# Kernel tuning notes

Hardware: AMD Instinct MI355X
Metric: run time of the kernel (lower is better)

The kernel has to match this reference:

```python
import jax, jax.numpy as jnp
import numpy as np

C = 256
HEADS = 8
HEAD_DIM = C // HEADS
GROUPS = 8
EPS = 1e-5


def setup_inputs() -> dict:
    key = jax.random.key(0)
    ks = jax.random.split(key, 11)
    B, S = 2, 16
    s = 0.02
    return {
        "x": jax.random.normal(ks[0], (B, C, S, S, S), dtype=jnp.float32),
        "gn_w": jnp.ones((C,), jnp.float32),
        "gn_b": jnp.zeros((C,), jnp.float32),
        "wq": jax.random.normal(ks[1], (C, C), jnp.float32) * s,
        "bq": jnp.zeros((C,), jnp.float32),
        "wk": jax.random.normal(ks[2], (C, C), jnp.float32) * s,
        "bk": jnp.zeros((C,), jnp.float32),
        "wv": jax.random.normal(ks[3], (C, C), jnp.float32) * s,
        "bv": jnp.zeros((C,), jnp.float32),
        "wo": jax.random.normal(ks[4], (C, C), jnp.float32) * s,
        "bo": jnp.zeros((C,), jnp.float32),
    }


def _group_norm(x, w, b):
    # x: [B, C, D, H, W]; GroupNorm(8, C) with affine params
    B, Cc, D, H, W = x.shape
    xg = x.reshape(B, GROUPS, Cc // GROUPS, D, H, W)
    mu = jnp.mean(xg, axis=(2, 3, 4, 5), keepdims=True)
    var = jnp.mean(jnp.square(xg - mu), axis=(2, 3, 4, 5), keepdims=True)
    xn = ((xg - mu) * jax.lax.rsqrt(var + EPS)).reshape(B, Cc, D, H, W)
    return xn * w[None, :, None, None, None] + b[None, :, None, None, None]


def reference(x, gn_w, gn_b, wq, bq, wk, bk, wv, bv, wo, bo):
    B, Cc, D, H, W = x.shape
    N = D * H * W
    xn = _group_norm(x, gn_w, gn_b).reshape(B, Cc, N)  # [B,C,N]
    # 1x1x1 Conv3d == per-voxel linear: weight [out,in]
    Q = jnp.einsum("oc,bcn->bon", wq, xn) + bq[None, :, None]
    K = jnp.einsum("oc,bcn->bon", wk, xn) + bk[None, :, None]
    V = jnp.einsum("oc,bcn->bon", wv, xn) + bv[None, :, None]
    Q = Q.reshape(B, HEADS, HEAD_DIM, N)
    K = K.reshape(B, HEADS, HEAD_DIM, N)
    V = V.reshape(B, HEADS, HEAD_DIM, N)
    scale = np.sqrt(HEAD_DIM).astype(np.float32)
    attn = jnp.einsum("bhdn,bhdm->bhnm", Q, K) / scale
    attn = jax.nn.softmax(attn, axis=-1)
    out = jnp.einsum("bhnm,bhdm->bhdn", attn, V)  # [B,h,hd,N]
    out = out.reshape(B, Cc, N)
    out = jnp.einsum("oc,bcn->bon", wo, out) + bo[None, :, None]
    return x + out.reshape(B, Cc, D, H, W)
```

## Files before the change

### kernel.cpp

```cpp
#include <hip/hip_runtime.h>

#define B_   2
#define C_   256
#define N_   4096
#define H_   8
#define HD_  32
#define G_   8
#define CPG_ 32

typedef short short8 __attribute__((ext_vector_type(8)));
typedef short short4v __attribute__((ext_vector_type(4)));
typedef unsigned uint4v __attribute__((ext_vector_type(4)));
typedef float f32x4  __attribute__((ext_vector_type(4)));
typedef float f4     __attribute__((ext_vector_type(4)));

__device__ __forceinline__ float b2f(short s) {
    return __uint_as_float(((unsigned)(unsigned short)s) << 16);
}
__device__ __forceinline__ short f2b(float f) {
    unsigned u = __float_as_uint(f);
    unsigned r = (u + 0x7FFF + ((u >> 16) & 1)) >> 16;
    return (short)r;
}

__global__ __launch_bounds__(256) void gn_part(const float* __restrict__ x,
                                               float* __restrict__ part) {
    int blk = blockIdx.x;
    const f4* p = (const f4*)x + (size_t)(blk >> 6) * (CPG_ * N_ / 4) + (size_t)(blk & 63) * 512;
    float s = 0.f, ss = 0.f;
#pragma unroll
    for (int i = 0; i < 2; i++) {
        f4 v = p[threadIdx.x + i * 256];
#pragma unroll
        for (int j = 0; j < 4; j++) { float f = v[j]; s += f; ss += f * f; }
    }
#pragma unroll
    for (int off = 32; off > 0; off >>= 1) {
        s  += __shfl_down(s, off);
        ss += __shfl_down(ss, off);
    }
    __shared__ float rs[4], rss[4];
    int w = threadIdx.x >> 6;
    if ((threadIdx.x & 63) == 0) { rs[w] = s; rss[w] = ss; }
    __syncthreads();
    if (threadIdx.x == 0) {
        part[blk * 2]     = rs[0] + rs[1] + rs[2] + rs[3];
        part[blk * 2 + 1] = rss[0] + rss[1] + rss[2] + rss[3];
    }
}

__global__ __launch_bounds__(256) void gemm_qkv(
    const float* __restrict__ x,
    const float* __restrict__ gw, const float* __restrict__ gb,
    const float* __restrict__ part,
    const float* __restrict__ wq, const float* __restrict__ bq,
    const float* __restrict__ wk, const float* __restrict__ bk,
    const float* __restrict__ wv, const float* __restrict__ bv,
    short* __restrict__ q, short* __restrict__ kt, short* __restrict__ v) {
    int z = blockIdx.z;
    int b = z / 3, which = z % 3;
    const float* W    = which == 0 ? wq : (which == 1 ? wk : wv);
    const float* bias = which == 0 ? bq : (which == 1 ? bk : bv);
    bool trans = (which != 2);
    float mul = (which == 0) ? (0.17677669529663687f * 1.4426950408889634f) : 1.0f;

    __shared__ short wl[64][40];
    __shared__ short xl[128][40];
    __shared__ float ga[256], gbb[256];
    __shared__ float mus[8], rstds[8];

    int o0 = blockIdx.y * 64, n0 = blockIdx.x * 128;
    int tid = threadIdx.x;
    int w = tid >> 6, lane = tid & 63, li = lane & 15, quad = lane >> 4;
    int wr = w & 1, wc = w >> 1;

#pragma unroll
    for (int gi = 0; gi < 2; gi++) {
        int g = w * 2 + gi;
        const float* pp = &part[(size_t)(b * 8 + g) * 128 + lane * 2];
        float s = pp[0], ss = pp[1];
#pragma unroll
        for (int off = 32; off > 0; off >>= 1) {
            s  += __shfl_down(s, off);
            ss += __shfl_down(ss, off);
        }
        if (lane == 0) {
            const float inv = 1.f / (float)(CPG_ * N_);
            float mu = s * inv;
            float var = ss * inv - mu * mu;
            mus[g] = mu;
            rstds[g] = rsqrtf(var + 1e-5f);
        }
    }
    __syncthreads();
    {
        int c = tid, g = c >> 5;
        float a = rstds[g] * gw[c];
        ga[c]  = a;
        gbb[c] = gb[c] - mus[g] * a;
    }

    f32x4 acc[8];
#pragma unroll
    for (int i = 0; i < 8; i++) acc[i] = (f32x4){0.f, 0.f, 0.f, 0.f};

    int cpair = tid >> 4, l16 = tid & 15;
    __syncthreads();

    for (int k0 = 0; k0 < 256; k0 += 32) {
        {
            int row = tid >> 2, co = (tid & 3) << 3;
            const float* wp = &W[(size_t)(o0 + row) * 256 + k0 + co];
            f4 wa = *(const f4*)wp;
            f4 wb = *(const f4*)(wp + 4);
            short8 w8;
#pragma unroll
            for (int j = 0; j < 4; j++) { w8[j] = f2b(wa[j]); w8[j + 4] = f2b(wb[j]); }
            *(short8*)&wl[row][co] = w8;
        }
        {
            int c0 = k0 + cpair * 2;
            float a0 = ga[c0],     b0c = gbb[c0];
            float a1 = ga[c0 + 1], b1c = gbb[c0 + 1];
            const float* xr0 = x + ((size_t)(b * 256 + c0)) * N_ + n0 + l16;
            const float* xr1 = xr0 + N_;
#pragma unroll
            for (int j = 0; j < 8; j++) {
                unsigned lo = (unsigned short)f2b(xr0[16 * j] * a0 + b0c);
                unsigned hi = (unsigned short)f2b(xr1[16 * j] * a1 + b1c);
                *(unsigned*)&xl[l16 + 16 * j][cpair * 2] = lo | (hi << 16);
            }
        }
        __syncthreads();
        short8 af[4], bfr[4];
        if (trans) {
#pragma unroll
            for (int i = 0; i < 4; i++) af[i]  = *(short8*)&xl[wr * 64 + i * 16 + li][quad * 8];
#pragma unroll
            for (int j = 0; j < 2; j++) bfr[j] = *(short8*)&wl[wc * 32 + j * 16 + li][quad * 8];
#pragma unroll
            for (int i = 0; i < 4; i++)
#pragma unroll
                for (int j = 0; j < 2; j++)
                    acc[i * 2 + j] = __builtin_amdgcn_mfma_f32_16x16x32_bf16(af[i], bfr[j], acc[i * 2 + j], 0, 0, 0);
        } else {
#pragma unroll
            for (int i = 0; i < 2; i++) af[i]  = *(short8*)&wl[wr * 32 + i * 16 + li][quad * 8];
#pragma unroll
            for (int j = 0; j < 4; j++) bfr[j] = *(short8*)&xl[wc * 64 + j * 16 + li][quad * 8];
#pragma unroll
            for (int i = 0; i < 2; i++)
#pragma unroll
                for (int j = 0; j < 4; j++)
                    acc[i * 4 + j] = __builtin_amdgcn_mfma_f32_16x16x32_bf16(af[i], bfr[j], acc[i * 4 + j], 0, 0, 0);
        }
        __syncthreads();
    }

    if (which == 2) {
        short* outp = v + (size_t)b * C_ * N_;
#pragma unroll
        for (int i = 0; i < 2; i++) {
            int ob = o0 + wr * 32 + i * 16 + quad * 4;
#pragma unroll
            for (int j = 0; j < 4; j++) {
                int n_ = n0 + wc * 64 + j * 16 + li;
#pragma unroll
                for (int r = 0; r < 4; r++) {
                    float val = acc[i * 4 + j][r] + bias[ob + r];
                    outp[(size_t)(ob + r) * N_ + n_] = f2b(val);
                }
            }
        }
    } else if (which == 0) {
        short* outp = q + (size_t)b * N_ * C_;
#pragma unroll
        for (int i = 0; i < 4; i++) {
            int nb_ = n0 + wr * 64 + i * 16 + quad * 4;
#pragma unroll
            for (int j = 0; j < 2; j++) {
                int o_ = o0 + wc * 32 + j * 16 + li;
                float bv_ = bias[o_];
#pragma unroll
                for (int r = 0; r < 4; r++)
                    outp[(size_t)(nb_ + r) * C_ + o_] = f2b((acc[i * 2 + j][r] + bv_) * mul);
            }
        }
    } else {
#pragma unroll
        for (int i = 0; i < 4; i++) {
            int nb_ = n0 + wr * 64 + i * 16 + quad * 4;
#pragma unroll
            for (int j = 0; j < 2; j++) {
                int o_ = o0 + wc * 32 + j * 16 + li;
                int hh = o_ >> 5, d = o_ & 31;
                float bv_ = bias[o_];
                short* kdst = kt + ((size_t)(b * 8 + hh) * N_) * HD_ + d;
#pragma unroll
                for (int r = 0; r < 4; r++)
                    kdst[(size_t)(nb_ + r) * HD_] = f2b(acc[i * 2 + j][r] + bv_);
            }
        }
    }
}

__global__ __launch_bounds__(512) void flash(const short* __restrict__ q,
                                             const short* __restrict__ ktp,
                                             const short* __restrict__ v,
                                             float* __restrict__ Opart,
                                             float* __restrict__ lrbuf) {
    int bid = blockIdx.x;
    int xcd = bid & 7;
    int rest = bid >> 3;
    int bh = xcd * 2 + (rest & 1);
    int r2 = rest >> 1;
    int nb = r2 & 15;
    int half = r2 >> 4;
    int b = bh >> 3, h = bh & 7;

    const short* QT = q   + (size_t)b * N_ * C_ + h * HD_;
    const short* KP = ktp + (size_t)bh * N_ * HD_ + (size_t)half * 2048 * HD_;
    const short* V  = v   + ((size_t)b * C_ + h * HD_) * N_ + half * 2048;
    float* Oh  = Opart + (size_t)half * B_ * N_ * C_ + (size_t)b * N_ * C_ + h * HD_;
    float* lrp = lrbuf + (size_t)half * 16 * N_ + (size_t)bh * N_;

    __shared__ short kl[2 * 2560];
    __shared__ short vl[2 * 2304];

    int tid = threadIdx.x, w = tid >> 6, lane = tid & 63, li = lane & 15, quad = lane >> 4;
    int n0w = nb * 256 + w * 32;

    short8 qf0 = *(const short8*)&QT[(size_t)(n0w + li) * 256 + quad * 8];
    short8 qf1 = *(const short8*)&QT[(size_t)(n0w + 16 + li) * 256 + quad * 8];

    f32x4 oa00 = (f32x4){0.f,0.f,0.f,0.f}, oa01 = oa00, oa10 = oa00, oa11 = oa00;
    float lr0 = 0.f, lr1 = 0.f;
    const f32x4 zero = (f32x4){0.f, 0.f, 0.f, 0.f};

    int krow = tid >> 3, kcol = (tid & 7) << 2;
    const short* kgp = KP + (size_t)krow * HD_ + kcol;
    int klo = krow * 40 + kcol;
    int vd = tid >> 4, g = tid & 15;
    int mbase = 32 * (g >> 3) + 16 * (g & 1) + 4 * ((g >> 1) & 3);
    const short* vgp = V + (size_t)vd * N_ + mbase;
    int vlo = vd * 72 + g * 4;

    short4v kst = *(const short4v*)kgp;
    short4v vst = *(const short4v*)vgp;

    f32x4 s0[4], s1[4];
    short8 vf[4];

    for (int t = 0; t < 32; ++t) {
        int buf = t & 1;
        *(short4v*)&kl[buf * 2560 + klo] = kst;
        *(short4v*)&vl[buf * 2304 + vlo] = vst;
        if (t < 31) {
            kst = *(const short4v*)(kgp + (size_t)(t + 1) * 64 * HD_);
            vst = *(const short4v*)(vgp + (t + 1) * 64);
        }
        __syncthreads();

        __builtin_amdgcn_s_setprio(1);
#pragma unroll
        for (int c = 0; c < 4; c++) {
            short8 kf = *(short8*)&kl[buf * 2560 + (c * 16 + li) * 40 + quad * 8];
            s0[c] = __builtin_amdgcn_mfma_f32_16x16x32_bf16(kf, qf0, zero, 0, 0, 0);
            s1[c] = __builtin_amdgcn_mfma_f32_16x16x32_bf16(kf, qf1, zero, 0, 0, 0);
        }
        __builtin_amdgcn_s_setprio(0);

        vf[0] = *(short8*)&vl[buf * 2304 + li * 72 + quad * 8];
        vf[1] = *(short8*)&vl[buf * 2304 + (16 + li) * 72 + quad * 8];
        vf[2] = *(short8*)&vl[buf * 2304 + li * 72 + 32 + quad * 8];
        vf[3] = *(short8*)&vl[buf * 2304 + (16 + li) * 72 + 32 + quad * 8];

        unsigned paw[8];
        float lp = 0.f;
#pragma unroll
        for (int c = 0; c < 4; c++) {
            float e0 = __builtin_amdgcn_exp2f(s0[c][0]);
            float e1 = __builtin_amdgcn_exp2f(s0[c][1]);
            float e2 = __builtin_amdgcn_exp2f(s0[c][2]);
            float e3 = __builtin_amdgcn_exp2f(s0[c][3]);
            lp += (e0 + e1) + (e2 + e3);
            paw[2 * c]     = __builtin_amdgcn_perm(__float_as_uint(e1), __float_as_uint(e0), 0x07060302);
            paw[2 * c + 1] = __builtin_amdgcn_perm(__float_as_uint(e3), __float_as_uint(e2), 0x07060302);
        }
        lr0 += lp;
        uint4v p0 = (uint4v){paw[0], paw[1], paw[2], paw[3]};
        uint4v p1 = (uint4v){paw[4], paw[5], paw[6], paw[7]};
        short8 a0 = __builtin_bit_cast(short8, p0);
        short8 a1 = __builtin_bit_cast(short8, p1);

        lp = 0.f;
#pragma unroll
        for (int c = 0; c < 4; c++) {
            float e0 = __builtin_amdgcn_exp2f(s1[c][0]);
            float e1 = __builtin_amdgcn_exp2f(s1[c][1]);
            float e2 = __builtin_amdgcn_exp2f(s1[c][2]);
            float e3 = __builtin_amdgcn_exp2f(s1[c][3]);
            lp += (e0 + e1) + (e2 + e3);
            paw[2 * c]     = __builtin_amdgcn_perm(__float_as_uint(e1), __float_as_uint(e0), 0x07060302);
            paw[2 * c + 1] = __builtin_amdgcn_perm(__float_as_uint(e3), __float_as_uint(e2), 0x07060302);
        }
        lr1 += lp;
        uint4v p2 = (uint4v){paw[0], paw[1], paw[2], paw[3]};
        uint4v p3 = (uint4v){paw[4], paw[5], paw[6], paw[7]};
        short8 a2 = __builtin_bit_cast(short8, p2);
        short8 a3 = __builtin_bit_cast(short8, p3);

        __builtin_amdgcn_s_setprio(1);
        oa00 = __builtin_amdgcn_mfma_f32_16x16x32_bf16(a0, vf[0], oa00, 0, 0, 0);
        oa01 = __builtin_amdgcn_mfma_f32_16x16x32_bf16(a0, vf[1], oa01, 0, 0, 0);
        oa00 = __builtin_amdgcn_mfma_f32_16x16x32_bf16(a1, vf[2], oa00, 0, 0, 0);
        oa01 = __builtin_amdgcn_mfma_f32_16x16x32_bf16(a1, vf[3], oa01, 0, 0, 0);
        oa10 = __builtin_amdgcn_mfma_f32_16x16x32_bf16(a2, vf[0], oa10, 0, 0, 0);
        oa11 = __builtin_amdgcn_mfma_f32_16x16x32_bf16(a2, vf[1], oa11, 0, 0, 0);
        oa10 = __builtin_amdgcn_mfma_f32_16x16x32_bf16(a3, vf[2], oa10, 0, 0, 0);
        oa11 = __builtin_amdgcn_mfma_f32_16x16x32_bf16(a3, vf[3], oa11, 0, 0, 0);
        __builtin_amdgcn_s_setprio(0);
    }

    lr0 += __shfl_xor(lr0, 16); lr0 += __shfl_xor(lr0, 32);
    lr1 += __shfl_xor(lr1, 16); lr1 += __shfl_xor(lr1, 32);
#pragma unroll
    for (int r = 0; r < 4; r++) {
        size_t n_ = (size_t)(n0w + quad * 4 + r);
        Oh[n_ * 256 + li]      = oa00[r];
        Oh[n_ * 256 + 16 + li] = oa01[r];
        size_t n2 = (size_t)(n0w + 16 + quad * 4 + r);
        Oh[n2 * 256 + li]      = oa10[r];
        Oh[n2 * 256 + 16 + li] = oa11[r];
    }
    if (quad == 0) {
        lrp[n0w + li]      = lr0;
        lrp[n0w + 16 + li] = lr1;
    }
}

__global__ __launch_bounds__(256) void combine(const float* __restrict__ Opart,
                                               const float* __restrict__ lrbuf,
                                               short* __restrict__ aoT) {
    int idx = blockIdx.x * 256 + threadIdx.x;
    int cg = idx & 31;
    int n  = (idx >> 5) & 4095;
    int b  = idx >> 17;
    int c0 = cg * 8;
    int bh = b * 8 + (c0 >> 5);
    float l = lrbuf[(size_t)bh * N_ + n] + lrbuf[(size_t)16 * N_ + (size_t)bh * N_ + n];
    float inv = 1.f / l;
    size_t base = ((size_t)b * N_ + n) * 256 + c0;
    const float* p0 = Opart + base;
    const float* p1 = Opart + (size_t)B_ * N_ * C_ + base;
    f4 x0 = *(const f4*)p0, x1 = *(const f4*)(p0 + 4);
    f4 y0 = *(const f4*)p1, y1 = *(const f4*)(p1 + 4);
    short8 r;
#pragma unroll
    for (int j = 0; j < 4; j++) {
        r[j]     = f2b((x0[j] + y0[j]) * inv);
        r[j + 4] = f2b((x1[j] + y1[j]) * inv);
    }
    *(short8*)&aoT[base] = r;
}

__global__ __launch_bounds__(256) void gemm_out(const float* __restrict__ W,
                                                const float* __restrict__ bias,
                                                const short* __restrict__ aoT,
                                                const float* __restrict__ resid,
                                                float* __restrict__ out) {
    int b = blockIdx.z;
    const short* X = aoT + (size_t)b * N_ * C_;
    const float* R = resid + (size_t)b * C_ * N_;
    float* outp = out + (size_t)b * C_ * N_;

    __shared__ short wl[128][40];
    __shared__ short xl[64][40];

    int o0 = blockIdx.y * 128, n0 = blockIdx.x * 64;
    int tid = threadIdx.x;
    int w = tid >> 6, lane = tid & 63, li = lane & 15, quad = lane >> 4;
    int wr = w & 1, wc = w >> 1;

    f32x4 acc[4][2];
#pragma unroll
    for (int i = 0; i < 4; i++)
#pragma unroll
        for (int j = 0; j < 2; j++) acc[i][j] = (f32x4){0.f, 0.f, 0.f, 0.f};

    for (int k0 = 0; k0 < 256; k0 += 32) {
#pragma unroll
        for (int i = 0; i < 2; i++) {
            int idx = tid + i * 256;
            int row = idx >> 2, co = (idx & 3) << 3;
            const float* wp = &W[(size_t)(o0 + row) * 256 + k0 + co];
            f4 wa = *(const f4*)wp;
            f4 wb = *(const f4*)(wp + 4);
            short8 w8;
#pragma unroll
            for (int j = 0; j < 4; j++) { w8[j] = f2b(wa[j]); w8[j + 4] = f2b(wb[j]); }
            *(short8*)&wl[row][co] = w8;
        }
        {
            int row = tid >> 2, co = (tid & 3) << 3;
            *(short8*)&xl[row][co] = *(const short8*)&X[(size_t)(n0 + row) * 256 + k0 + co];
        }
        __syncthreads();
        short8 af[4], bfr[2];
#pragma unroll
        for (int i = 0; i < 4; i++) af[i]  = *(short8*)&wl[wr * 64 + i * 16 + li][quad * 8];
#pragma unroll
        for (int j = 0; j < 2; j++) bfr[j] = *(short8*)&xl[wc * 32 + j * 16 + li][quad * 8];
#pragma unroll
        for (int i = 0; i < 4; i++)
#pragma unroll
            for (int j = 0; j < 2; j++)
                acc[i][j] = __builtin_amdgcn_mfma_f32_16x16x32_bf16(af[i], bfr[j], acc[i][j], 0, 0, 0);
        __syncthreads();
    }
#pragma unroll
    for (int i = 0; i < 4; i++) {
        int ob = o0 + wr * 64 + i * 16 + quad * 4;
#pragma unroll
        for (int j = 0; j < 2; j++) {
            int n_ = n0 + wc * 32 + j * 16 + li;
#pragma unroll
            for (int r = 0; r < 4; r++) {
                size_t idx = (size_t)(ob + r) * N_ + n_;
                outp[idx] = acc[i][j][r] + bias[ob + r] + R[idx];
            }
        }
    }
}

extern "C" void kernel_launch(void* const* d_in, const int* in_sizes, int n_in,
                              void* d_out, int out_size, void* d_ws, size_t ws_size,
                              hipStream_t stream) {
    const float* x  = (const float*)d_in[0];
    const float* gw = (const float*)d_in[1];
    const float* gb = (const float*)d_in[2];
    const float* wq = (const float*)d_in[3];
    const float* bq = (const float*)d_in[4];
    const float* wk = (const float*)d_in[5];
    const float* bk = (const float*)d_in[6];
    const float* wv = (const float*)d_in[7];
    const float* bv = (const float*)d_in[8];
    const float* wo = (const float*)d_in[9];
    const float* bo = (const float*)d_in[10];
    float* out = (float*)d_out;

    char* ws = (char*)d_ws;
    float* part = (float*)ws;
    const size_t TS = (size_t)B_ * N_ * C_;
    short* aoT = (short*)(ws + 16384);
    short* q   = aoT + TS;
    short* kt  = q + TS;
    short* v   = kt + TS;
    float* Of  = (float*)(v + TS);
    float* lr  = Of + 2 * TS;

    gn_part<<<1024, 256, 0, stream>>>(x, part);
    gemm_qkv<<<dim3(32, 4, 6), 256, 0, stream>>>(x, gw, gb, part,
                                                 wq, bq, wk, bk, wv, bv, q, kt, v);
    flash<<<512, 512, 0, stream>>>(q, kt, v, Of, lr);
    combine<<<1024, 256, 0, stream>>>(Of, lr, aoT);
    gemm_out<<<dim3(64, 2, 2), 256, 0, stream>>>(wo, bo, aoT, x, out);
}
```

Baseline: 149.8 us.

## Drop split-KV combine pass and normalize in flash; shrink gemm_out tile

The flash kernel no longer splits the key range in two. Each block now walks all 64 key tiles and normalizes by the row sum itself, writing bf16 attention output directly, which removes the combine kernel and the fp32 partial-output round trip. The flash grid halves to 256 blocks, so parallelism and occupancy drop while the serial loop per block doubles. Separately, gemm_out's output-channel tile is halved from 128 to 64, doubling its grid for more blocks in flight.

```diff
diff --git a/kernel.cpp b/kernel.cpp
--- a/kernel.cpp
+++ b/kernel.cpp
@@ -207,22 +207,18 @@
 __global__ __launch_bounds__(512) void flash(const short* __restrict__ q,
                                              const short* __restrict__ ktp,
                                              const short* __restrict__ v,
-                                             float* __restrict__ Opart,
-                                             float* __restrict__ lrbuf) {
+                                             short* __restrict__ aoT) {
     int bid = blockIdx.x;
     int xcd = bid & 7;
     int rest = bid >> 3;
     int bh = xcd * 2 + (rest & 1);
-    int r2 = rest >> 1;
-    int nb = r2 & 15;
-    int half = r2 >> 4;
+    int nb = rest >> 1;
     int b = bh >> 3, h = bh & 7;
 
     const short* QT = q   + (size_t)b * N_ * C_ + h * HD_;
-    const short* KP = ktp + (size_t)bh * N_ * HD_ + (size_t)half * 2048 * HD_;
-    const short* V  = v   + ((size_t)b * C_ + h * HD_) * N_ + half * 2048;
-    float* Oh  = Opart + (size_t)half * B_ * N_ * C_ + (size_t)b * N_ * C_ + h * HD_;
-    float* lrp = lrbuf + (size_t)half * 16 * N_ + (size_t)bh * N_;
+    const short* KP = ktp + (size_t)bh * N_ * HD_;
+    const short* V  = v   + ((size_t)b * C_ + h * HD_) * N_;
+    short* O = aoT + (size_t)b * N_ * C_ + h * HD_;
 
     __shared__ short kl[2 * 2560];
     __shared__ short vl[2 * 2304];
@@ -251,11 +247,11 @@
     f32x4 s0[4], s1[4];
     short8 vf[4];
 
-    for (int t = 0; t < 32; ++t) {
+    for (int t = 0; t < 64; ++t) {
         int buf = t & 1;
         *(short4v*)&kl[buf * 2560 + klo] = kst;
         *(short4v*)&vl[buf * 2304 + vlo] = vst;
-        if (t < 31) {
+        if (t < 63) {
             kst = *(const short4v*)(kgp + (size_t)(t + 1) * 64 * HD_);
             vst = *(const short4v*)(vgp + (t + 1) * 64);
         }
@@ -326,42 +322,17 @@
     lr1 += __shfl_xor(lr1, 16); lr1 += __shfl_xor(lr1, 32);
 #pragma unroll
     for (int r = 0; r < 4; r++) {
+        float ln0 = __shfl(lr0, quad * 4 + r);
+        float inv0 = 1.f / ln0;
         size_t n_ = (size_t)(n0w + quad * 4 + r);
-        Oh[n_ * 256 + li]      = oa00[r];
-        Oh[n_ * 256 + 16 + li] = oa01[r];
+        O[n_ * 256 + li]      = f2b(oa00[r] * inv0);
+        O[n_ * 256 + 16 + li] = f2b(oa01[r] * inv0);
+        float ln1 = __shfl(lr1, quad * 4 + r);
+        float inv1 = 1.f / ln1;
         size_t n2 = (size_t)(n0w + 16 + quad * 4 + r);
-        Oh[n2 * 256 + li]      = oa10[r];
-        Oh[n2 * 256 + 16 + li] = oa11[r];
-    }
-    if (quad == 0) {
-        lrp[n0w + li]      = lr0;
-        lrp[n0w + 16 + li] = lr1;
-    }
-}
-
-__global__ __launch_bounds__(256) void combine(const float* __restrict__ Opart,
-                                               const float* __restrict__ lrbuf,
-                                               short* __restrict__ aoT) {
-    int idx = blockIdx.x * 256 + threadIdx.x;
-    int cg = idx & 31;
-    int n  = (idx >> 5) & 4095;
-    int b  = idx >> 17;
-    int c0 = cg * 8;
-    int bh = b * 8 + (c0 >> 5);
-    float l = lrbuf[(size_t)bh * N_ + n] + lrbuf[(size_t)16 * N_ + (size_t)bh * N_ + n];
-    float inv = 1.f / l;
-    size_t base = ((size_t)b * N_ + n) * 256 + c0;
-    const float* p0 = Opart + base;
-    const float* p1 = Opart + (size_t)B_ * N_ * C_ + base;
-    f4 x0 = *(const f4*)p0, x1 = *(const f4*)(p0 + 4);
-    f4 y0 = *(const f4*)p1, y1 = *(const f4*)(p1 + 4);
-    short8 r;
-#pragma unroll
-    for (int j = 0; j < 4; j++) {
-        r[j]     = f2b((x0[j] + y0[j]) * inv);
-        r[j + 4] = f2b((x1[j] + y1[j]) * inv);
-    }
-    *(short8*)&aoT[base] = r;
+        O[n2 * 256 + li]      = f2b(oa10[r] * inv1);
+        O[n2 * 256 + 16 + li] = f2b(oa11[r] * inv1);
+    }
 }
 
 __global__ __launch_bounds__(256) void gemm_out(const float* __restrict__ W,
@@ -374,25 +345,23 @@
     const float* R = resid + (size_t)b * C_ * N_;
     float* outp = out + (size_t)b * C_ * N_;
 
-    __shared__ short wl[128][40];
+    __shared__ short wl[64][40];
     __shared__ short xl[64][40];
 
-    int o0 = blockIdx.y * 128, n0 = blockIdx.x * 64;
+    int o0 = blockIdx.y * 64, n0 = blockIdx.x * 64;
     int tid = threadIdx.x;
     int w = tid >> 6, lane = tid & 63, li = lane & 15, quad = lane >> 4;
     int wr = w & 1, wc = w >> 1;
 
-    f32x4 acc[4][2];
-#pragma unroll
-    for (int i = 0; i < 4; i++)
+    f32x4 acc[2][2];
+#pragma unroll
+    for (int i = 0; i < 2; i++)
 #pragma unroll
         for (int j = 0; j < 2; j++) acc[i][j] = (f32x4){0.f, 0.f, 0.f, 0.f};
 
+    int row = tid >> 2, co = (tid & 3) << 3;
     for (int k0 = 0; k0 < 256; k0 += 32) {
-#pragma unroll
-        for (int i = 0; i < 2; i++) {
-            int idx = tid + i * 256;
-            int row = idx >> 2, co = (idx & 3) << 3;
+        {
             const float* wp = &W[(size_t)(o0 + row) * 256 + k0 + co];
             f4 wa = *(const f4*)wp;
             f4 wb = *(const f4*)(wp + 4);
@@ -401,26 +370,23 @@
             for (int j = 0; j < 4; j++) { w8[j] = f2b(wa[j]); w8[j + 4] = f2b(wb[j]); }
             *(short8*)&wl[row][co] = w8;
         }
-        {
-            int row = tid >> 2, co = (tid & 3) << 3;
-            *(short8*)&xl[row][co] = *(const short8*)&X[(size_t)(n0 + row) * 256 + k0 + co];
-        }
+        *(short8*)&xl[row][co] = *(const short8*)&X[(size_t)(n0 + row) * 256 + k0 + co];
         __syncthreads();
-        short8 af[4], bfr[2];
-#pragma unroll
-        for (int i = 0; i < 4; i++) af[i]  = *(short8*)&wl[wr * 64 + i * 16 + li][quad * 8];
+        short8 af[2], bfr[2];
+#pragma unroll
+        for (int i = 0; i < 2; i++) af[i]  = *(short8*)&wl[wr * 32 + i * 16 + li][quad * 8];
 #pragma unroll
         for (int j = 0; j < 2; j++) bfr[j] = *(short8*)&xl[wc * 32 + j * 16 + li][quad * 8];
 #pragma unroll
-        for (int i = 0; i < 4; i++)
+        for (int i = 0; i < 2; i++)
 #pragma unroll
             for (int j = 0; j < 2; j++)
                 acc[i][j] = __builtin_amdgcn_mfma_f32_16x16x32_bf16(af[i], bfr[j], acc[i][j], 0, 0, 0);
         __syncthreads();
     }
 #pragma unroll
-    for (int i = 0; i < 4; i++) {
-        int ob = o0 + wr * 64 + i * 16 + quad * 4;
+    for (int i = 0; i < 2; i++) {
+        int ob = o0 + wr * 32 + i * 16 + quad * 4;
 #pragma unroll
         for (int j = 0; j < 2; j++) {
             int n_ = n0 + wc * 32 + j * 16 + li;
@@ -456,13 +422,10 @@
     short* q   = aoT + TS;
     short* kt  = q + TS;
     short* v   = kt + TS;
-    float* Of  = (float*)(v + TS);
-    float* lr  = Of + 2 * TS;
 
     gn_part<<<1024, 256, 0, stream>>>(x, part);
     gemm_qkv<<<dim3(32, 4, 6), 256, 0, stream>>>(x, gw, gb, part,
                                                  wq, bq, wk, bk, wv, bv, q, kt, v);
-    flash<<<512, 512, 0, stream>>>(q, kt, v, Of, lr);
-    combine<<<1024, 256, 0, stream>>>(Of, lr, aoT);
-    gemm_out<<<dim3(64, 2, 2), 256, 0, stream>>>(wo, bo, aoT, x, out);
-}
+    flash<<<256, 512, 0, stream>>>(q, kt, v, aoT);
+    gemm_out<<<dim3(64, 4, 2), 256, 0, stream>>>(wo, bo, aoT, x, out);
+}
```

Result: no change. 150.0 us (+0.2%).
